# Performance work log

Measured on AMD Instinct MI355X. Metric: run time of the kernel, lower is better.

The kernel has to match this reference:

```python
import jax, jax.numpy as jnp
import numpy as np

N_FFT = 800
HOP = 200
WIN = 800
FREQ = N_FFT // 2 + 1  # 401
B, T = 32, 480000


def _make_weights():
    # periodic hann window
    n = np.arange(N_FFT)
    window = 0.5 - 0.5 * np.cos(2.0 * np.pi * np.arange(WIN) / WIN)
    k = np.arange(FREQ)
    angle = 2.0 * np.pi * np.outer(k, n) / N_FFT  # [FREQ, N_FFT]
    fwd_real = (np.cos(angle) * window).astype(np.float32)
    fwd_imag = (-np.sin(angle) * window).astype(np.float32)
    angle_t = 2.0 * np.pi * np.outer(n, k) / N_FFT  # [N_FFT, FREQ]
    inv_window = window * (1.0 / N_FFT)
    bwd_real = (np.cos(angle_t).T * inv_window).astype(np.float32)  # [FREQ, N_FFT]
    bwd_imag = (np.sin(angle_t).T * inv_window).astype(np.float32)
    return (jnp.asarray(fwd_real), jnp.asarray(fwd_imag),
            jnp.asarray(bwd_real), jnp.asarray(bwd_imag))


def setup_inputs() -> dict:
    key = jax.random.key(0)
    x = jax.random.normal(key, (B, T), dtype=jnp.float32)
    wfr, wfi, wbr, wbi = _make_weights()
    return {"x": x, "w_fwd_real": wfr, "w_fwd_imag": wfi,
            "w_bwd_real": wbr, "w_bwd_imag": wbi}


def reference(x, w_fwd_real, w_fwd_imag, w_bwd_real, w_bwd_imag):
    Tlen = x.shape[-1]
    pad = N_FFT // 2
    xp = jnp.pad(x, ((0, 0), (pad, pad)), mode="edge")  # replicate pad
    n_frames = (xp.shape[-1] - N_FFT) // HOP + 1
    # frame extraction (== conv1d stride HOP with dense DFT kernels)
    fidx = jnp.arange(n_frames)[:, None] * HOP + jnp.arange(N_FFT)[None, :]
    frames = xp[:, fidx]  # [B, F, N_FFT]
    real = jnp.einsum("bfn,kn->bkf", frames, w_fwd_real)  # [B, FREQ, F]
    imag = jnp.einsum("bfn,kn->bkf", frames, w_fwd_imag)
    magnitude = jnp.sqrt(real * real + imag * imag + 1e-14)
    phase = jnp.arctan2(imag, real)
    phase = jnp.where((imag == 0) & (real < 0), jnp.pi, phase)
    # inverse: iDFT-as-GEMM + overlap-add (== conv_transpose1d stride HOP)
    rp = magnitude * jnp.cos(phase)
    ip = magnitude * jnp.sin(phase)
    yr = jnp.einsum("bkf,kn->bfn", rp, w_bwd_real)  # [B, F, N_FFT]
    yi = jnp.einsum("bkf,kn->bfn", ip, w_bwd_imag)
    y_frames = yr - yi
    l_out = (n_frames - 1) * HOP + N_FFT
    oidx = jnp.arange(n_frames)[:, None] * HOP + jnp.arange(N_FFT)[None, :]
    wave = jnp.zeros((x.shape[0], l_out), dtype=x.dtype).at[:, oidx].add(y_frames)
    return wave[:, pad:pad + Tlen]
```

## Files before the change

### kernel.cpp

```cpp
#include <hip/hip_runtime.h>
#include <math.h>

#define NFFT    800
#define HOP     200
#define NB      32
#define TLEN    480000
#define NFRAMES 2401
#define NSEGG   2404
#define QPB     16
#define NQB     (TLEN / HOP / QPB)

#define DLT  0.00785398163397448f
#define C1K  0.99996915760f
#define S1K  0.00785390090f
#define C2K  0.99987663248f
#define S2K  0.01570731731f
#define C3K  0.99972243010f
#define S3K  0.02355976470f


__global__ __launch_bounds__(256) void seg_partials(const float* __restrict__ x,
                                                    float* __restrict__ P) {
    const int wave = threadIdx.x >> 6;
    const int lane = threadIdx.x & 63;
    const int sg = blockIdx.x * 4 + wave;
    const int b  = sg / NSEGG;
    const int g  = sg - b * NSEGG - 2;
    const float* xb = x + (size_t)b * TLEN;

    float p1e = 0.f, p1o = 0.f, pce = 0.f, pco = 0.f, pse = 0.f, pso = 0.f;
    if (lane < 50) {
        float4 v;
        if (g >= 0 && g <= 2399) {
            v = ((const float4*)(xb + 200 * g))[lane];
        } else {
            const float xv = (g < 0) ? xb[0] : xb[TLEN - 1];
            v = make_float4(xv, xv, xv, xv);
        }
        const int gm = (g + 4) & 3;
        const int tm = gm * 200 + 4 * lane;
        float s0, c0;
        __sincosf((float)tm * DLT, &s0, &c0);
        const float c1 = c0 * C1K - s0 * S1K, s1 = s0 * C1K + c0 * S1K;
        const float c2 = c0 * C2K - s0 * S2K, s2 = s0 * C2K + c0 * S2K;
        const float c3 = c0 * C3K - s0 * S3K, s3 = s0 * C3K + c0 * S3K;
        p1e = v.x + v.z;            p1o = v.y + v.w;
        pce = c0 * v.x + c2 * v.z;  pco = c1 * v.y + c3 * v.w;
        pse = s0 * v.x + s2 * v.z;  pso = s1 * v.y + s3 * v.w;
    }
    for (int m = 1; m < 64; m <<= 1) {
        p1e += __shfl_xor(p1e, m);  p1o += __shfl_xor(p1o, m);
        pce += __shfl_xor(pce, m);  pco += __shfl_xor(pco, m);
        pse += __shfl_xor(pse, m);  pso += __shfl_xor(pso, m);
    }
    if (lane == 0) {
        float* r = P + (size_t)sg * 6;
        ((float2*)r)[0] = make_float2(p1e, p1o);
        ((float2*)r)[1] = make_float2(pce, pco);
        ((float2*)r)[2] = make_float2(pse, pso);
    }
}

__global__ __launch_bounds__(256) void synth(const float* __restrict__ x,
                                             const float* __restrict__ P,
                                             float* __restrict__ out) {
    __shared__ float  stage[22 * 6];
    __shared__ float4 segc[2][QPB];
    __shared__ float  sfs[2][19];

    const int qb = blockIdx.x;
    const int b  = blockIdx.y;
    const int q0 = qb * QPB;

    if (threadIdx.x < 22 * 6) {
        int g = q0 - 3 + (int)(threadIdx.x / 6);
        g = min(max(g, -2), 2401);
        stage[threadIdx.x] = P[(size_t)(b * NSEGG + g + 2) * 6 + threadIdx.x % 6];
    }
    __syncthreads();

    const bool slowb = (qb == 0) || (qb == NQB - 1);

    if (!slowb) {
        if (threadIdx.x < 2 * QPB) {
            const int par = threadIdx.x & 1;
            const int ql  = threadIdx.x >> 1;
            const int q   = q0 + ql;
            float A = 0.f, C = 0.f, D = 0.f;
            for (int f = q - 1; f <= q + 2; ++f) {
                const int s0i = (f - 2) - (q0 - 3);
                float sp1 = 0.f, spc = 0.f, sps = 0.f;
#pragma unroll
                for (int k = 0; k < 4; ++k) {
                    const float* rec = &stage[(s0i + k) * 6];
                    sp1 += rec[par];  spc += rec[2 + par];  sps += rec[4 + par];
                }
                const int fm = f & 3;
                const float tr = (fm == 0) ? spc : (fm == 1) ? sps : (fm == 2) ? -spc : -sps;
                const float S = 0.5f * sp1 + 0.5f * tr;
                A += S;
                if (fm == 0) C += S; else if (fm == 2) C -= S;
                else if (fm == 1) D += S; else D -= S;
            }
            segc[par][ql] = make_float4(A * (1.0f / 1600.0f),
                                        sqrtf(C * C + D * D) * (1.0f / 1600.0f),
                                        atan2f(D, C), 0.f);
        }
        __syncthreads();

        const float4* xg4 = (const float4*)(x + (size_t)b * TLEN + HOP * q0);
        float4* og4 = (float4*)(out + (size_t)b * TLEN + HOP * q0);
        const int pmb = (q0 & 3) * 200 + 400;
        for (int j = threadIdx.x; j < 50 * QPB; j += 256) {
            const float4 xv = xg4[j];
            const int sl = j / 50;
            const float4 ce = segc[0][sl];
            const float4 co = segc[1][sl];
            const int pm = (pmb + 4 * j) % 800;
            const float xa[4] = {xv.x, xv.y, xv.z, xv.w};
            float r[4];
#pragma unroll
            for (int c = 0; c < 4; ++c) {
                const float4 cc = (c & 1) ? co : ce;
                r[c] = 0.75f * xa[c] + cc.x - cc.y * __cosf((float)(pm + c) * DLT - cc.z);
            }
            og4[j] = make_float4(r[0], r[1], r[2], r[3]);
        }
    } else {
        if (threadIdx.x < 38) {
            const int par = threadIdx.x & 1;
            const int fl  = threadIdx.x >> 1;
            const int f   = q0 - 1 + fl;
            float S = 0.f;
            if (f >= 0 && f < NFRAMES) {
                const int s0i = (f - 2) - (q0 - 3);
                float sp1 = 0.f, spc = 0.f, sps = 0.f;
#pragma unroll
                for (int k = 0; k < 4; ++k) {
                    const float* rec = &stage[(s0i + k) * 6];
                    sp1 += rec[par];  spc += rec[2 + par];  sps += rec[4 + par];
                }
                const int fm = f & 3;
                const float tr = (fm == 0) ? spc : (fm == 1) ? sps : (fm == 2) ? -spc : -sps;
                S = 0.5f * sp1 + 0.5f * tr;
            }
            sfs[par][fl] = S;
        }
        __syncthreads();

        const float4* xg4 = (const float4*)(x + (size_t)b * TLEN + HOP * q0);
        float4* og4 = (float4*)(out + (size_t)b * TLEN + HOP * q0);
        for (int j = threadIdx.x; j < 50 * QPB; j += 256) {
            const float4 xv = xg4[j];
            const float xa[4] = {xv.x, xv.y, xv.z, xv.w};
            float r[4];
            const int pbase = HOP * q0 + 4 * j + 400;
#pragma unroll
            for (int c = 0; c < 4; ++c) {
                const int p = pbase + c;
                int fhi = p / HOP;
                if (fhi > NFRAMES - 1) fhi = NFRAMES - 1;
                const int flo = (p >= NFFT) ? (p - NFFT) / HOP + 1 : 0;
                const int par = p & 1;
                float acc = 0.f;
                for (int f = flo; f <= fhi; ++f) {
                    const int n = p - HOP * f;
                    const float w = 0.5f - 0.5f * __cosf((float)n * DLT);
                    acc += w * (0.5f * w * xa[c] + (1.0f / 800.0f) * sfs[par][f - (q0 - 1)]);
                }
                r[c] = acc;
            }
            og4[j] = make_float4(r[0], r[1], r[2], r[3]);
        }
    }
}

extern "C" void kernel_launch(void* const* d_in, const int* in_sizes, int n_in,
                              void* d_out, int out_size, void* d_ws, size_t ws_size,
                              hipStream_t stream) {
    const float* x = (const float*)d_in[0];
    float* out = (float*)d_out;
    float* P   = (float*)d_ws;

    seg_partials<<<dim3(NB * NSEGG / 4), dim3(256), 0, stream>>>(x, P);
    synth<<<dim3(NQB, NB), dim3(256), 0, stream>>>(x, P, out);
}
```

Before: 144.9 us.

## Fuse segment partial sums into synthesis kernel and simplify boundary blocks

Merges the two-kernel pipeline into one kernel: each block recomputes the per-segment partial sums for its 22 neighboring segments in shared memory, so the workspace write/read round trip and the second launch go away. Edge blocks now reuse the fast closed-form path and apply a small analytic correction to the first or last segment instead of running a per-sample frame loop. In exchange, blocks overlapping neighbors redundantly reload about 22/16 of their input and recompute shared partials, and the sin/cos recurrence via rotation may add small rounding drift.

New measurement: 122.7 us. 15.3% less time.

```diff
diff --git a/kernel.cpp b/kernel.cpp
--- a/kernel.cpp
+++ b/kernel.cpp
@@ -1,14 +1,12 @@
 #include <hip/hip_runtime.h>
 #include <math.h>
 
-#define NFFT    800
 #define HOP     200
 #define NB      32
 #define TLEN    480000
-#define NFRAMES 2401
-#define NSEGG   2404
 #define QPB     16
 #define NQB     (TLEN / HOP / QPB)
+#define NSEGP   22
 
 #define DLT  0.00785398163397448f
 #define C1K  0.99996915760f
@@ -17,161 +15,126 @@
 #define S2K  0.01570731731f
 #define C3K  0.99972243010f
 #define S3K  0.02355976470f
+#define C40  0.95105651629515f
+#define S40  0.30901699437495f
 
-
-__global__ __launch_bounds__(256) void seg_partials(const float* __restrict__ x,
-                                                    float* __restrict__ P) {
-    const int wave = threadIdx.x >> 6;
-    const int lane = threadIdx.x & 63;
-    const int sg = blockIdx.x * 4 + wave;
-    const int b  = sg / NSEGG;
-    const int g  = sg - b * NSEGG - 2;
-    const float* xb = x + (size_t)b * TLEN;
-
-    float p1e = 0.f, p1o = 0.f, pce = 0.f, pco = 0.f, pse = 0.f, pso = 0.f;
-    if (lane < 50) {
-        float4 v;
-        if (g >= 0 && g <= 2399) {
-            v = ((const float4*)(xb + 200 * g))[lane];
-        } else {
-            const float xv = (g < 0) ? xb[0] : xb[TLEN - 1];
-            v = make_float4(xv, xv, xv, xv);
-        }
-        const int gm = (g + 4) & 3;
-        const int tm = gm * 200 + 4 * lane;
-        float s0, c0;
-        __sincosf((float)tm * DLT, &s0, &c0);
-        const float c1 = c0 * C1K - s0 * S1K, s1 = s0 * C1K + c0 * S1K;
-        const float c2 = c0 * C2K - s0 * S2K, s2 = s0 * C2K + c0 * S2K;
-        const float c3 = c0 * C3K - s0 * S3K, s3 = s0 * C3K + c0 * S3K;
-        p1e = v.x + v.z;            p1o = v.y + v.w;
-        pce = c0 * v.x + c2 * v.z;  pco = c1 * v.y + c3 * v.w;
-        pse = s0 * v.x + s2 * v.z;  pso = s1 * v.y + s3 * v.w;
-    }
-    for (int m = 1; m < 64; m <<= 1) {
-        p1e += __shfl_xor(p1e, m);  p1o += __shfl_xor(p1o, m);
-        pce += __shfl_xor(pce, m);  pco += __shfl_xor(pco, m);
-        pse += __shfl_xor(pse, m);  pso += __shfl_xor(pso, m);
-    }
-    if (lane == 0) {
-        float* r = P + (size_t)sg * 6;
-        ((float2*)r)[0] = make_float2(p1e, p1o);
-        ((float2*)r)[1] = make_float2(pce, pco);
-        ((float2*)r)[2] = make_float2(pse, pso);
-    }
-}
-
-__global__ __launch_bounds__(256) void synth(const float* __restrict__ x,
-                                             const float* __restrict__ P,
-                                             float* __restrict__ out) {
-    __shared__ float  stage[22 * 6];
+__global__ __launch_bounds__(256) void stft_one(const float* __restrict__ x,
+                                                float* __restrict__ out) {
+    __shared__ float  part[NSEGP][10][6];
+    __shared__ float  pg[NSEGP][6];
     __shared__ float4 segc[2][QPB];
-    __shared__ float  sfs[2][19];
 
     const int qb = blockIdx.x;
     const int b  = blockIdx.y;
     const int q0 = qb * QPB;
+    const float* xb = x + (size_t)b * TLEN;
 
-    if (threadIdx.x < 22 * 6) {
-        int g = q0 - 3 + (int)(threadIdx.x / 6);
-        g = min(max(g, -2), 2401);
-        stage[threadIdx.x] = P[(size_t)(b * NSEGG + g + 2) * 6 + threadIdx.x % 6];
+    if (threadIdx.x < NSEGP * 10) {
+        const int s = threadIdx.x / 10;
+        const int k = threadIdx.x - 10 * s;
+        const int g = q0 - 3 + s;
+        const int gm = (g + 4) & 3;
+        float c0, s0;
+        __sincosf((float)(gm * 200 + 4 * k) * DLT, &s0, &c0);
+        float p1e = 0.f, p1o = 0.f, pce = 0.f, pco = 0.f, pse = 0.f, pso = 0.f;
+        const bool inb = (g >= 0) && (g <= 2399);
+        float4 ve;
+        if (!inb) {
+            const float xe = (g < 0) ? xb[0] : xb[TLEN - 1];
+            ve = make_float4(xe, xe, xe, xe);
+        }
+#pragma unroll
+        for (int i = 0; i < 5; ++i) {
+            float4 v;
+            if (inb) v = ((const float4*)(xb + 200 * g))[k + 10 * i];
+            else     v = ve;
+            const float c1 = c0 * C1K - s0 * S1K, s1 = s0 * C1K + c0 * S1K;
+            const float c2 = c0 * C2K - s0 * S2K, s2 = s0 * C2K + c0 * S2K;
+            const float c3 = c0 * C3K - s0 * S3K, s3 = s0 * C3K + c0 * S3K;
+            p1e += v.x + v.z;            p1o += v.y + v.w;
+            pce += c0 * v.x + c2 * v.z;  pco += c1 * v.y + c3 * v.w;
+            pse += s0 * v.x + s2 * v.z;  pso += s1 * v.y + s3 * v.w;
+            const float cn = c0 * C40 - s0 * S40;
+            s0 = s0 * C40 + c0 * S40;  c0 = cn;
+        }
+        part[s][k][0] = p1e;  part[s][k][1] = p1o;
+        part[s][k][2] = pce;  part[s][k][3] = pco;
+        part[s][k][4] = pse;  part[s][k][5] = pso;
     }
     __syncthreads();
 
-    const bool slowb = (qb == 0) || (qb == NQB - 1);
+    if (threadIdx.x < NSEGP * 6) {
+        const int s = threadIdx.x / 6;
+        const int c = threadIdx.x - 6 * s;
+        float a = 0.f;
+#pragma unroll
+        for (int k = 0; k < 10; ++k) a += part[s][k][c];
+        pg[s][c] = a;
+    }
+    __syncthreads();
 
-    if (!slowb) {
-        if (threadIdx.x < 2 * QPB) {
-            const int par = threadIdx.x & 1;
-            const int ql  = threadIdx.x >> 1;
-            const int q   = q0 + ql;
-            float A = 0.f, C = 0.f, D = 0.f;
-            for (int f = q - 1; f <= q + 2; ++f) {
-                const int s0i = (f - 2) - (q0 - 3);
-                float sp1 = 0.f, spc = 0.f, sps = 0.f;
+    if (threadIdx.x < 2 * QPB) {
+        const int par = threadIdx.x & 1;
+        const int ql  = threadIdx.x >> 1;
+        const int q   = q0 + ql;
+        float A = 0.f, C = 0.f, D = 0.f;
 #pragma unroll
-                for (int k = 0; k < 4; ++k) {
-                    const float* rec = &stage[(s0i + k) * 6];
-                    sp1 += rec[par];  spc += rec[2 + par];  sps += rec[4 + par];
-                }
-                const int fm = f & 3;
-                const float tr = (fm == 0) ? spc : (fm == 1) ? sps : (fm == 2) ? -spc : -sps;
-                const float S = 0.5f * sp1 + 0.5f * tr;
-                A += S;
-                if (fm == 0) C += S; else if (fm == 2) C -= S;
-                else if (fm == 1) D += S; else D -= S;
+        for (int df = -1; df <= 2; ++df) {
+            const int f = q + df;
+            if (f < 0 || f > 2400) continue;
+            const int ls0 = f - q0 + 1;
+            float sp1 = 0.f, spc = 0.f, sps = 0.f;
+#pragma unroll
+            for (int kk = 0; kk < 4; ++kk) {
+                const float* rec = pg[ls0 + kk];
+                sp1 += rec[par];  spc += rec[2 + par];  sps += rec[4 + par];
             }
-            segc[par][ql] = make_float4(A * (1.0f / 1600.0f),
-                                        sqrtf(C * C + D * D) * (1.0f / 1600.0f),
-                                        atan2f(D, C), 0.f);
+            const int fm = f & 3;
+            const float tr = (fm == 0) ? spc : (fm == 1) ? sps : (fm == 2) ? -spc : -sps;
+            const float S = 0.5f * sp1 + 0.5f * tr;
+            A += S;
+            if (fm == 0) C += S; else if (fm == 2) C -= S;
+            else if (fm == 1) D += S; else D -= S;
         }
-        __syncthreads();
+        segc[par][ql] = make_float4(A * (1.0f / 1600.0f),
+                                    sqrtf(C * C + D * D) * (1.0f / 1600.0f),
+                                    atan2f(D, C), 0.f);
+    }
+    __syncthreads();
 
-        const float4* xg4 = (const float4*)(x + (size_t)b * TLEN + HOP * q0);
-        float4* og4 = (float4*)(out + (size_t)b * TLEN + HOP * q0);
-        const int pmb = (q0 & 3) * 200 + 400;
-        for (int j = threadIdx.x; j < 50 * QPB; j += 256) {
-            const float4 xv = xg4[j];
-            const int sl = j / 50;
-            const float4 ce = segc[0][sl];
-            const float4 co = segc[1][sl];
-            const int pm = (pmb + 4 * j) % 800;
-            const float xa[4] = {xv.x, xv.y, xv.z, xv.w};
-            float r[4];
+    const bool headblk = (qb == 0);
+    const bool tailblk = (qb == NQB - 1);
+    const float4* xg4 = (const float4*)(xb + HOP * q0);
+    float4* og4 = (float4*)(out + (size_t)b * TLEN + HOP * q0);
+    const int pmb = (q0 & 3) * 200 + 400;
+    for (int j = threadIdx.x; j < 50 * QPB; j += 256) {
+        const float4 xv = xg4[j];
+        const int sl = j / 50;
+        const float4 ce = segc[0][sl];
+        const float4 co = segc[1][sl];
+        const int pm = (pmb + 4 * j) % 800;
+        const float xa[4] = {xv.x, xv.y, xv.z, xv.w};
+        float r[4];
+#pragma unroll
+        for (int c = 0; c < 4; ++c) {
+            const float4 cc = (c & 1) ? co : ce;
+            r[c] = 0.75f * xa[c] + cc.x - cc.y * __cosf((float)(pm + c) * DLT - cc.z);
+        }
+        if (headblk && sl == 0) {
 #pragma unroll
             for (int c = 0; c < 4; ++c) {
-                const float4 cc = (c & 1) ? co : ce;
-                r[c] = 0.75f * xa[c] + cc.x - cc.y * __cosf((float)(pm + c) * DLT - cc.z);
+                const float wm = 0.5f + 0.5f * __sinf((float)(pm + c) * DLT);
+                r[c] -= 0.5f * wm * wm * xa[c];
             }
-            og4[j] = make_float4(r[0], r[1], r[2], r[3]);
         }
-    } else {
-        if (threadIdx.x < 38) {
-            const int par = threadIdx.x & 1;
-            const int fl  = threadIdx.x >> 1;
-            const int f   = q0 - 1 + fl;
-            float S = 0.f;
-            if (f >= 0 && f < NFRAMES) {
-                const int s0i = (f - 2) - (q0 - 3);
-                float sp1 = 0.f, spc = 0.f, sps = 0.f;
-#pragma unroll
-                for (int k = 0; k < 4; ++k) {
-                    const float* rec = &stage[(s0i + k) * 6];
-                    sp1 += rec[par];  spc += rec[2 + par];  sps += rec[4 + par];
-                }
-                const int fm = f & 3;
-                const float tr = (fm == 0) ? spc : (fm == 1) ? sps : (fm == 2) ? -spc : -sps;
-                S = 0.5f * sp1 + 0.5f * tr;
-            }
-            sfs[par][fl] = S;
-        }
-        __syncthreads();
-
-        const float4* xg4 = (const float4*)(x + (size_t)b * TLEN + HOP * q0);
-        float4* og4 = (float4*)(out + (size_t)b * TLEN + HOP * q0);
-        for (int j = threadIdx.x; j < 50 * QPB; j += 256) {
-            const float4 xv = xg4[j];
-            const float xa[4] = {xv.x, xv.y, xv.z, xv.w};
-            float r[4];
-            const int pbase = HOP * q0 + 4 * j + 400;
+        if (tailblk && sl == QPB - 1) {
 #pragma unroll
             for (int c = 0; c < 4; ++c) {
-                const int p = pbase + c;
-                int fhi = p / HOP;
-                if (fhi > NFRAMES - 1) fhi = NFRAMES - 1;
-                const int flo = (p >= NFFT) ? (p - NFFT) / HOP + 1 : 0;
-                const int par = p & 1;
-                float acc = 0.f;
-                for (int f = flo; f <= fhi; ++f) {
-                    const int n = p - HOP * f;
-                    const float w = 0.5f - 0.5f * __cosf((float)n * DLT);
-                    acc += w * (0.5f * w * xa[c] + (1.0f / 800.0f) * sfs[par][f - (q0 - 1)]);
-                }
-                r[c] = acc;
+                const float wm = 0.5f - 0.5f * __sinf((float)(pm + c) * DLT);
+                r[c] -= 0.5f * wm * wm * xa[c];
             }
-            og4[j] = make_float4(r[0], r[1], r[2], r[3]);
         }
+        og4[j] = make_float4(r[0], r[1], r[2], r[3]);
     }
 }
 
@@ -180,8 +143,5 @@
                               hipStream_t stream) {
     const float* x = (const float*)d_in[0];
     float* out = (float*)d_out;
-    float* P   = (float*)d_ws;
-
-    seg_partials<<<dim3(NB * NSEGG / 4), dim3(256), 0, stream>>>(x, P);
-    synth<<<dim3(NQB, NB), dim3(256), 0, stream>>>(x, P, out);
+    stft_one<<<dim3(NQB, NB), dim3(256), 0, stream>>>(x, out);
 }
```
